# Kernel optimization log

Hardware: AMD Instinct MI355X
Metric: run time of the kernel (lower is better)

The kernel has to match this reference:

```python
import jax, jax.numpy as jnp
import numpy as np
from jax.scipy.linalg import expm, solve_triangular

B, N, K, A, V = 2, 256, 16, 16, 32000
ALPHA = 1.0
LAMBDA_BELIEF = 1.0
EPS = 1e-8   # kl_divergence jitter
EPS2 = 1e-6  # pairwise-KL jitter


def _spd(key, b, n, k, scale=0.3):
    a = jax.random.normal(key, (b, n, k, k)) * scale
    return jnp.einsum('bnkl,bnml->bnkm', a, a) + jnp.eye(k)


def setup_inputs() -> dict:
    key = jax.random.key(0)
    ks = jax.random.split(key, 9)
    mu = jax.random.normal(ks[0], (B, N, K))
    Sigma = _spd(ks[1], B, N, K)
    phi = jax.random.normal(ks[2], (B, N, A)) * 0.05
    mu_prior = jax.random.normal(ks[3], (B, N, K))
    Sigma_prior = _spd(ks[4], B, N, K)
    beta = jax.random.uniform(ks[5], (B, N, N)) / N
    W_out = jax.random.normal(ks[6], (V, K)) * 0.02
    R = jax.random.normal(ks[7], (A, K, K))
    generators = (R - jnp.swapaxes(R, -1, -2)) * 0.1  # skew-symmetric Lie generators
    targets = jax.random.randint(ks[8], (B, N), 0, V)
    return {"mu": mu, "Sigma": Sigma, "phi": phi, "mu_prior": mu_prior,
            "Sigma_prior": Sigma_prior, "beta": beta, "W_out": W_out,
            "generators": generators, "targets": targets}


def _bexpm(M):
    # batched matrix exponential over leading dims
    shape = M.shape
    return jax.vmap(expm)(M.reshape(-1, shape[-2], shape[-1])).reshape(shape)


def _potential(mu, Sigma, phi, mu_prior, Sigma_prior, beta, W_out, generators, targets):
    I = jnp.eye(K, dtype=mu.dtype)

    # --- V_self: alpha * sum_n KL(q_n || p_n), explicit-inverse formulation ---
    Sq = Sigma + EPS * I
    Sp = Sigma_prior + EPS * I
    Sp_inv = jnp.linalg.inv(Sp)
    trace_t = jnp.einsum('bnij,bnji->bn', Sp_inv, Sq)
    dmu = mu_prior - mu
    mahal = jnp.einsum('bni,bnij,bnj->bn', dmu, Sp_inv, dmu)
    logdet = jnp.linalg.slogdet(Sp)[1] - jnp.linalg.slogdet(Sq)[1]
    kl_self = 0.5 * (trace_t + mahal - K + logdet)
    V_self = ALPHA * kl_self.sum(-1)

    # --- V_align: pairwise KL under Lie transport Omega_ij = e^{phi_i G} e^{-phi_j G} ---
    phi_mat = jnp.einsum('bna,aij->bnij', phi, generators)          # (B,N,K,K)
    exp_phi = _bexpm(phi_mat)
    exp_neg_phi = _bexpm(-phi_mat)
    Omega = jnp.einsum('bikl,bjlm->bijkm', exp_phi, exp_neg_phi)    # (B,N,N,K,K)
    mu_t = jnp.einsum('bijkl,bjl->bijk', Omega, mu)                 # (B,N,N,K)
    # Omega Sigma_j Omega^T (congruence -> SPD)
    Sigma_t = jnp.einsum('bijkl,bjlm,bijnm->bijkn', Omega, Sigma, Omega)

    Stp = Sigma_t + EPS2 * I
    L_p = jnp.linalg.cholesky(Stp)                                  # (B,N,N,K,K)
    Sigma_i = jnp.broadcast_to((Sigma + EPS2 * I)[:, :, None], (B, N, N, K, K))
    Y = solve_triangular(L_p, Sigma_i, lower=True)
    Z = solve_triangular(jnp.swapaxes(L_p, -1, -2), Y, lower=False)
    trace_term = jnp.diagonal(Z, axis1=-2, axis2=-1).sum(-1)        # (B,N,N)

    delta = mu_t - mu[:, :, None, :]
    v = solve_triangular(L_p, delta[..., None], lower=True)[..., 0]
    mahal_term = (v ** 2).sum(-1)

    logdet_p = 2.0 * jnp.log(jnp.diagonal(L_p, axis1=-2, axis2=-1) + EPS2).sum(-1)
    L_q = jnp.linalg.cholesky(Sigma + EPS2 * I)                     # (B,N,K,K)
    logdet_q = 2.0 * jnp.log(jnp.diagonal(L_q, axis1=-2, axis2=-1) + EPS2).sum(-1)

    kl_all = 0.5 * (trace_term + mahal_term - K + logdet_p - logdet_q[:, :, None])
    kl_all = jnp.maximum(kl_all, 0.0)
    kl_all = kl_all * (1.0 - jnp.eye(N, dtype=mu.dtype))            # zero diagonal
    V_align = LAMBDA_BELIEF * (beta * kl_all).sum((-2, -1))

    # --- V_ce: cross entropy over W_out projection of mu ---
    logits = jnp.einsum('bnk,vk->bnv', mu, W_out)
    logp = jax.nn.log_softmax(logits, axis=-1)
    ce = -jnp.take_along_axis(logp, targets[..., None], axis=-1)[..., 0]
    V_ce = ce.sum(-1)

    return V_self + V_align + V_ce


def reference(mu, Sigma, phi, mu_prior, Sigma_prior, beta, W_out, generators, targets):
    return _potential(mu, Sigma, phi, mu_prior, Sigma_prior, beta, W_out, generators, targets)
```

## Files before the change

kernel.cpp:

```cpp
#include <hip/hip_runtime.h>
#include <math.h>

#define NB 2
#define NN 256
#define KD 16
#define VV 32000
#define EPS_SELF 1e-8f
#define EPS_AL   1e-6f
#define NNODES (NB*NN)

#define CE_ROWS 8
#define CE_CH   32
#define CE_CHUNK (VV/CE_CH)

#define OFF_MT  0
#define OFF_SH  (NNODES*16)
#define OFF_P   (OFF_SH + NNODES*256)
#define OFF_LD  (OFF_P + NNODES*256)
#define OFF_KLS (OFF_LD + NNODES)
#define OFF_AP  (OFF_KLS + NNODES)
#define OFF_CEP (OFF_AP + NNODES)
#define OFF_CNT (OFF_CEP + NNODES*CE_CH)
#define WS_FLOATS (OFF_CNT + 4)

#define WAVE_SYNC() asm volatile("s_waitcnt lgkmcnt(0)" ::: "memory")

__device__ __forceinline__ void ld4(float* dst, const float4 v) {
  dst[0] = v.x; dst[1] = v.y; dst[2] = v.z; dst[3] = v.w;
}

__device__ __forceinline__ float dot16a(const float* a, const float* b) {
  float acc = 0.f;
  #pragma unroll
  for (int j = 0; j < 16; ++j) acc = fmaf(a[j], b[j], acc);
  return acc;
}

__device__ __forceinline__ void gj16(float aq[4], const int g, const int c, float* ldacc) {
  #pragma unroll
  for (int k = 0; k < 16; ++k) {
    float d    = __shfl(aq[k & 3], ((k >> 2) << 4) | k);
    float rowk = __shfl(aq[k & 3], ((k >> 2) << 4) | c);
    float ck[4];
    #pragma unroll
    for (int q = 0; q < 4; ++q) ck[q] = __shfl(aq[q], (g << 4) | k);
    if (ldacc) *ldacc += logf(d);
    float dinv = 1.f / d;
    #pragma unroll
    for (int q = 0; q < 4; ++q) {
      int r = 4*g + q;
      float vgen = fmaf(-ck[q] * dinv, rowk, aq[q]);
      aq[q] = (r == k) ? ((c == k) ? dinv : aq[q] * dinv)
                       : ((c == k) ? (-ck[q] * dinv) : vgen);
    }
  }
}

template<int QUIRK>
__device__ __forceinline__ float ge16_logdet(float aq[4], const int g, const int c) {
  float ld = 0.f;
  #pragma unroll
  for (int k = 0; k < 16; ++k) {
    float d    = __shfl(aq[k & 3], ((k >> 2) << 4) | k);
    float rowk = __shfl(aq[k & 3], ((k >> 2) << 4) | c);
    float ck[4];
    #pragma unroll
    for (int q = 0; q < 4; ++q) ck[q] = __shfl(aq[q], (g << 4) | k);
    ld += QUIRK ? 2.f * logf(sqrtf(d) + EPS_AL) : logf(d);
    float dinv = 1.f / d;
    #pragma unroll
    for (int q = 0; q < 4; ++q) {
      int r = 4*g + q;
      float upd = fmaf(-ck[q] * dinv, rowk, aq[q]);
      aq[q] = (r > k && c > k) ? upd : aq[q];
    }
  }
  return ld;
}

#define DOT16(q0,q1,q2,q3,A) \
  fmaf(q0.x,A[0],fmaf(q0.y,A[1],fmaf(q0.z,A[2],fmaf(q0.w,A[3], \
  fmaf(q1.x,A[4],fmaf(q1.y,A[5],fmaf(q1.z,A[6],fmaf(q1.w,A[7], \
  fmaf(q2.x,A[8],fmaf(q2.y,A[9],fmaf(q2.z,A[10],fmaf(q2.w,A[11], \
  fmaf(q3.x,A[12],fmaf(q3.y,A[13],fmaf(q3.z,A[14],q3.w*A[15])))))))))))))))

__global__ __launch_bounds__(256) void fusedA_kernel(
    const float* __restrict__ mu, const float* __restrict__ Sigma,
    const float* __restrict__ phi, const float* __restrict__ mu_prior,
    const float* __restrict__ Sigma_prior, const float* __restrict__ gen,
    const float* __restrict__ W, float* __restrict__ ws)
{
  __shared__ __align__(16) float smem[4][980];
  const int tid = threadIdx.x;
  const int bid = blockIdx.x;

  if (bid < 256) {
    if (bid == 0 && tid == 0) *(unsigned*)(ws + OFF_CNT) = 0u;
    const int w = tid >> 6, l = tid & 63;
    const int g = l >> 4, c = l & 15;
    const int unit = bid * 4 + w;
    const int role = unit & 1, node = unit >> 1;
    float* COLp = &smem[w][0];
    float* ROWp = &smem[w][320];
    float* AUXp = &smem[w][640];

    if (role == 0) {
      float phis[16];
      {
        const float4* p4 = (const float4*)(phi + node*16);
        ld4(phis, p4[0]); ld4(phis+4, p4[1]); ld4(phis+8, p4[2]); ld4(phis+12, p4[3]);
      }
      float x[4] = {0.f, 0.f, 0.f, 0.f};
      #pragma unroll
      for (int aa = 0; aa < 16; ++aa) {
        float4 gq = *(const float4*)(gen + aa*256 + c*16 + 4*g);
        x[0] = fmaf(phis[aa], gq.x, x[0]);
        x[1] = fmaf(phis[aa], gq.y, x[1]);
        x[2] = fmaf(phis[aa], gq.z, x[2]);
        x[3] = fmaf(phis[aa], gq.w, x[3]);
      }
      #pragma unroll
      for (int q = 0; q < 4; ++q) x[q] *= -0.125f;

      #pragma unroll
      for (int q = 0; q < 4; ++q) ROWp[(4*g+q)*20 + c] = x[q];
      WAVE_SYNC();
      float Mrow[4][16];
      #pragma unroll
      for (int q = 0; q < 4; ++q)
        #pragma unroll
        for (int j4 = 0; j4 < 4; ++j4)
          ld4(&Mrow[q][4*j4], *(const float4*)&ROWp[(4*g+q)*20 + 4*j4]);

      float t[4];
      #pragma unroll
      for (int q = 0; q < 4; ++q) t[q] = ((4*g+q) == c ? 1.f : 0.f) + x[q]*0.125f;
      for (int k = 7; k >= 1; --k) {
        *(float4*)&COLp[c*20 + 4*g] = make_float4(t[0], t[1], t[2], t[3]);
        WAVE_SYNC();
        float T[16];
        #pragma unroll
        for (int j4 = 0; j4 < 4; ++j4) ld4(&T[4*j4], *(const float4*)&COLp[c*20 + 4*j4]);
        #pragma unroll
        for (int q = 0; q < 4; ++q)
          t[q] = ((4*g+q) == c ? 1.f : 0.f) + dot16a(Mrow[q], T) / (float)k;
      }
      for (int s = 0; s < 3; ++s) {
        *(float4*)&COLp[c*20 + 4*g] = make_float4(t[0], t[1], t[2], t[3]);
        #pragma unroll
        for (int q = 0; q < 4; ++q) ROWp[(4*g+q)*20 + c] = t[q];
        WAVE_SYNC();
        float T[16];
        #pragma unroll
        for (int j4 = 0; j4 < 4; ++j4) ld4(&T[4*j4], *(const float4*)&COLp[c*20 + 4*j4]);
        float nt[4];
        #pragma unroll
        for (int q = 0; q < 4; ++q) {
          float acc = 0.f;
          #pragma unroll
          for (int j4 = 0; j4 < 4; ++j4) {
            float4 rv = *(const float4*)&ROWp[(4*g+q)*20 + 4*j4];
            acc = fmaf(rv.x, T[4*j4+0], acc);
            acc = fmaf(rv.y, T[4*j4+1], acc);
            acc = fmaf(rv.z, T[4*j4+2], acc);
            acc = fmaf(rv.w, T[4*j4+3], acc);
          }
          nt[q] = acc;
        }
        #pragma unroll
        for (int q = 0; q < 4; ++q) t[q] = nt[q];
      }
      *(float4*)&COLp[c*20 + 4*g] = make_float4(t[0], t[1], t[2], t[3]);
      WAVE_SYNC();
      float Ecol[16];
      #pragma unroll
      for (int j4 = 0; j4 < 4; ++j4) ld4(&Ecol[4*j4], *(const float4*)&COLp[c*20 + 4*j4]);

      float w1q[4];
      #pragma unroll
      for (int q = 0; q < 4; ++q) {
        float S[16];
        const float4* s4 = (const float4*)(Sigma + node*256 + (4*g+q)*16);
        ld4(S, s4[0]); ld4(S+4, s4[1]); ld4(S+8, s4[2]); ld4(S+12, s4[3]);
        w1q[q] = dot16a(S, Ecol);
      }
      *(float4*)&AUXp[c*20 + 4*g] = make_float4(w1q[0], w1q[1], w1q[2], w1q[3]);
      WAVE_SYNC();
      float W1c[16];
      #pragma unroll
      for (int j4 = 0; j4 < 4; ++j4) ld4(&W1c[4*j4], *(const float4*)&AUXp[c*20 + 4*j4]);

      float sh[4];
      #pragma unroll
      for (int q = 0; q < 4; ++q) {
        float Er[16];
        #pragma unroll
        for (int j4 = 0; j4 < 4; ++j4) ld4(&Er[4*j4], *(const float4*)&COLp[(4*g+q)*20 + 4*j4]);
        sh[q] = dot16a(Er, W1c) + ((4*g+q) == c ? EPS_AL : 0.f);
      }
      *(float4*)(ws + OFF_SH + node*256 + c*16 + 4*g) = make_float4(sh[0], sh[1], sh[2], sh[3]);

      {
        float muv[16];
        const float4* m4 = (const float4*)(mu + node*16);
        ld4(muv, m4[0]); ld4(muv+4, m4[1]); ld4(muv+8, m4[2]); ld4(muv+12, m4[3]);
        float mt = dot16a(Ecol, muv);
        if (g == 0) ws[OFF_MT + node*16 + c] = mt;
      }
      gj16(sh, g, c, (float*)nullptr);
      *(float4*)(ws + OFF_P + node*256 + c*16 + 4*g) = make_float4(sh[0], sh[1], sh[2], sh[3]);
    } else {
      float sp[4];
      {
        float4 v = *(const float4*)(Sigma_prior + node*256 + c*16 + 4*g);
        sp[0] = v.x + ((4*g+0 == c) ? EPS_SELF : 0.f);
        sp[1] = v.y + ((4*g+1 == c) ? EPS_SELF : 0.f);
        sp[2] = v.z + ((4*g+2 == c) ? EPS_SELF : 0.f);
        sp[3] = v.w + ((4*g+3 == c) ? EPS_SELF : 0.f);
      }
      float ldSp = 0.f;
      gj16(sp, g, c, &ldSp);

      float dmur[4], dmuc;
      {
        float4 a = *(const float4*)(mu_prior + node*16 + 4*g);
        float4 b = *(const float4*)(mu + node*16 + 4*g);
        dmur[0] = a.x - b.x; dmur[1] = a.y - b.y; dmur[2] = a.z - b.z; dmur[3] = a.w - b.w;
        dmuc = mu_prior[node*16 + c] - mu[node*16 + c];
      }
      float4 sv = *(const float4*)(Sigma + node*256 + c*16 + 4*g);
      float val = 0.f;
      {
        float s0 = sv.x + ((4*g+0 == c) ? EPS_SELF : 0.f);
        float s1 = sv.y + ((4*g+1 == c) ? EPS_SELF : 0.f);
        float s2 = sv.z + ((4*g+2 == c) ? EPS_SELF : 0.f);
        float s3 = sv.w + ((4*g+3 == c) ? EPS_SELF : 0.f);
        val = fmaf(sp[0], s0 + dmur[0]*dmuc, val);
        val = fmaf(sp[1], s1 + dmur[1]*dmuc, val);
        val = fmaf(sp[2], s2 + dmur[2]*dmuc, val);
        val = fmaf(sp[3], s3 + dmur[3]*dmuc, val);
      }
      #pragma unroll
      for (int o = 32; o; o >>= 1) val += __shfl_xor(val, o);

      float sq[4];
      sq[0] = sv.x + ((4*g+0 == c) ? EPS_SELF : 0.f);
      sq[1] = sv.y + ((4*g+1 == c) ? EPS_SELF : 0.f);
      sq[2] = sv.z + ((4*g+2 == c) ? EPS_SELF : 0.f);
      sq[3] = sv.w + ((4*g+3 == c) ? EPS_SELF : 0.f);
      float ldSq = ge16_logdet<0>(sq, g, c);
      float sg[4];
      sg[0] = sv.x + ((4*g+0 == c) ? EPS_AL : 0.f);
      sg[1] = sv.y + ((4*g+1 == c) ? EPS_AL : 0.f);
      sg[2] = sv.z + ((4*g+2 == c) ? EPS_AL : 0.f);
      sg[3] = sv.w + ((4*g+3 == c) ? EPS_AL : 0.f);
      float ldq = ge16_logdet<1>(sg, g, c);
      if (l == 0) {
        ws[OFF_KLS + node] = 0.5f * (val - 16.f + ldSp - ldSq);
        ws[OFF_LD + node]  = ldq;
      }
    }
  } else {
    const int idx = bid - 256;
    const int grp = idx & 63;
    const int ch  = idx >> 6;
    const int row0 = grp * CE_ROWS;
    float* mu_s = &smem[0][0];
    float* wred = &smem[0][128];

    if (tid < CE_ROWS*16) mu_s[tid] = mu[row0*16 + tid];
    __syncthreads();

    float A[CE_ROWS][16];
    #pragma unroll
    for (int r = 0; r < CE_ROWS; ++r)
      #pragma unroll
      for (int k = 0; k < 16; ++k) A[r][k] = mu_s[r*16+k];

    float acc[CE_ROWS];
    #pragma unroll
    for (int r = 0; r < CE_ROWS; ++r) acc[r] = 0.f;

    const float4* W4 = (const float4*)W;
    const int v0 = ch * CE_CHUNK;
    for (int v = v0 + tid; v < v0 + CE_CHUNK; v += 256) {
      float4 q0 = W4[v*4+0], q1 = W4[v*4+1], q2 = W4[v*4+2], q3 = W4[v*4+3];
      #pragma unroll
      for (int r = 0; r < CE_ROWS; ++r) {
        float lg = DOT16(q0,q1,q2,q3,A[r]);
        acc[r] += __expf(lg);
      }
    }
    #pragma unroll
    for (int r = 0; r < CE_ROWS; ++r)
      #pragma unroll
      for (int o = 32; o; o >>= 1) acc[r] += __shfl_xor(acc[r], o);
    const int w = tid >> 6, l = tid & 63;
    if (l == 0) {
      #pragma unroll
      for (int r = 0; r < CE_ROWS; ++r) wred[w*CE_ROWS + r] = acc[r];
    }
    __syncthreads();
    if (tid < CE_ROWS)
      ws[OFF_CEP + (row0 + tid)*CE_CH + ch] =
          wred[tid] + wred[CE_ROWS + tid] + wred[2*CE_ROWS + tid] + wred[3*CE_ROWS + tid];
  }
}

#define PSTR 260
__global__ __launch_bounds__(256) void alignB_kernel(
    const float* __restrict__ beta, const float* __restrict__ mu,
    const float* __restrict__ W, const int* __restrict__ targets,
    float* __restrict__ ws, float* __restrict__ out)
{
  __shared__ __align__(16) float ShI[16*PSTR];
  __shared__ __align__(16) float PJ[16*PSTR];
  __shared__ float mtI[256], mtJ[256], ldI[16], ldJ[16], red[4];
  __shared__ int lastflag;
  const int tid = threadIdx.x;
  const int ti = tid & 15, tj = tid >> 4;
  const int bx = blockIdx.x & 15, by = (blockIdx.x >> 4) & 15, bz = blockIdx.x >> 8;
  const int nodeI0 = bz*256 + by*16, nodeJ0 = bz*256 + bx*16;

  for (int idx = tid; idx < 16*256; idx += 256) {
    int row = idx >> 8, col = idx & 255;
    ShI[row*PSTR + col] = ws[OFF_SH + (nodeI0 + row)*256 + col];
    PJ [row*PSTR + col] = ws[OFF_P  + (nodeJ0 + row)*256 + col];
  }
  mtI[tid] = ws[OFF_MT + nodeI0*16 + tid];
  mtJ[tid] = ws[OFF_MT + nodeJ0*16 + tid];
  if (tid < 16) { ldI[tid] = ws[OFF_LD + nodeI0 + tid]; ldJ[tid] = ws[OFF_LD + nodeJ0 + tid]; }
  __syncthreads();

  const float4* si4 = (const float4*)&ShI[ti*PSTR];
  const float4* pj4 = (const float4*)&PJ[tj*PSTR];
  float tr = 0.f;
  #pragma unroll 16
  for (int t = 0; t < 64; ++t) {
    float4 xv = si4[t], yv = pj4[t];
    tr = fmaf(xv.x, yv.x, tr);
    tr = fmaf(xv.y, yv.y, tr);
    tr = fmaf(xv.z, yv.z, tr);
    tr = fmaf(xv.w, yv.w, tr);
  }

  const float* pj = &PJ[tj*PSTR];
  float d[16];
  #pragma unroll
  for (int k = 0; k < 16; ++k) d[k] = mtJ[tj*16+k] - mtI[ti*16+k];
  float mah = 0.f;
  #pragma unroll
  for (int k = 0; k < 16; ++k) {
    float acc = 0.f;
    #pragma unroll
    for (int ll = 0; ll < 16; ++ll) acc = fmaf(pj[k*16+ll], d[ll], acc);
    mah = fmaf(d[k], acc, mah);
  }

  float kl = 0.5f * (tr + mah - 16.f + ldJ[tj] - ldI[ti]);
  kl = fmaxf(kl, 0.f);
  int gi = by*16 + ti, gj = bx*16 + tj;
  float contrib = (gi == gj) ? 0.f : kl * beta[bz*65536 + gi*256 + gj];
  #pragma unroll
  for (int o = 32; o; o >>= 1) contrib += __shfl_down(contrib, o);
  __syncthreads();
  if ((tid & 63) == 0) red[tid >> 6] = contrib;
  __syncthreads();
  if (tid == 0) {
    ws[OFF_AP + (bz*16 + by)*16 + bx] = red[0] + red[1] + red[2] + red[3];
    unsigned old = __hip_atomic_fetch_add((unsigned*)(ws + OFF_CNT), 1u,
                                          __ATOMIC_ACQ_REL, __HIP_MEMORY_SCOPE_AGENT);
    lastflag = (old == 511u);
  }
  __syncthreads();

  if (lastflag) {
    double* dred = (double*)ShI;
    double v[2];
    #pragma unroll
    for (int b = 0; b < 2; ++b) {
      int row = b*256 + tid;
      float s = 0.f;
      #pragma unroll
      for (int c2 = 0; c2 < CE_CH; ++c2) s += ws[OFF_CEP + row*CE_CH + c2];
      int t = targets[row];
      float dt = 0.f;
      const float4* wt4 = (const float4*)(W + t*16);
      const float4* mr4 = (const float4*)(mu + row*16);
      #pragma unroll
      for (int j4 = 0; j4 < 4; ++j4) {
        float4 a = mr4[j4], bb = wt4[j4];
        dt = fmaf(a.x, bb.x, dt); dt = fmaf(a.y, bb.y, dt);
        dt = fmaf(a.z, bb.z, dt); dt = fmaf(a.w, bb.w, dt);
      }
      double ce = (double)logf(s) - (double)dt;
      v[b] = (double)ws[OFF_KLS + row] + (double)ws[OFF_AP + row] + ce;
    }
    for (int b = 0; b < 2; ++b) {
      dred[tid] = v[b];
      __syncthreads();
      for (int h = 128; h > 0; h >>= 1) {
        if (tid < h) dred[tid] += dred[tid + h];
        __syncthreads();
      }
      if (tid == 0) out[b] = (float)dred[0];
      __syncthreads();
    }
  }
}

extern "C" void kernel_launch(void* const* d_in, const int* in_sizes, int n_in,
                              void* d_out, int out_size, void* d_ws, size_t ws_size,
                              hipStream_t stream) {
  const float* mu          = (const float*)d_in[0];
  const float* Sigma       = (const float*)d_in[1];
  const float* phi         = (const float*)d_in[2];
  const float* mu_prior    = (const float*)d_in[3];
  const float* Sigma_prior = (const float*)d_in[4];
  const float* beta        = (const float*)d_in[5];
  const float* W_out       = (const float*)d_in[6];
  const float* gen         = (const float*)d_in[7];
  const int*   targets     = (const int*)d_in[8];
  float* out = (float*)d_out;
  float* ws  = (float*)d_ws;
  if (ws_size < (size_t)WS_FLOATS * sizeof(float)) return;

  fusedA_kernel<<<256 + (NNODES/CE_ROWS)*CE_CH, 256, 0, stream>>>(
      mu, Sigma, phi, mu_prior, Sigma_prior, gen, W_out, ws);
  alignB_kernel<<<NB*16*16, 256, 0, stream>>>(beta, mu, W_out, targets, ws, out);
}
```

Measured before the change: 44.32 us.

## Fold pairwise Mahalanobis term into trace via precomputed rank-one and projections

```diff
diff --git a/kernel.cpp b/kernel.cpp
--- a/kernel.cpp
+++ b/kernel.cpp
@@ -14,12 +14,14 @@
 #define CE_CHUNK (VV/CE_CH)
 
 #define OFF_MT  0
-#define OFF_SH  (NNODES*16)
-#define OFF_P   (OFF_SH + NNODES*256)
+#define OFF_O   (NNODES*16)
+#define OFF_P   (OFF_O + NNODES*256)
 #define OFF_LD  (OFF_P + NNODES*256)
 #define OFF_KLS (OFF_LD + NNODES)
 #define OFF_AP  (OFF_KLS + NNODES)
-#define OFF_CEP (OFF_AP + NNODES)
+#define OFF_Y   (OFF_AP + NNODES)
+#define OFF_W   (OFF_Y + NNODES*16)
+#define OFF_CEP (OFF_W + NNODES)
 #define OFF_CNT (OFF_CEP + NNODES*CE_CH)
 #define WS_FLOATS (OFF_CNT + 4)
 
@@ -34,6 +36,10 @@
   #pragma unroll
   for (int j = 0; j < 16; ++j) acc = fmaf(a[j], b[j], acc);
   return acc;
+}
+
+__device__ __forceinline__ float dot4(float4 a, float4 b) {
+  return fmaf(a.x, b.x, fmaf(a.y, b.y, fmaf(a.z, b.z, a.w * b.w)));
 }
 
 __device__ __forceinline__ void gj16(float aq[4], const int g, const int c, float* ldacc) {
@@ -78,13 +84,7 @@
   return ld;
 }
 
-#define DOT16(q0,q1,q2,q3,A) \
-  fmaf(q0.x,A[0],fmaf(q0.y,A[1],fmaf(q0.z,A[2],fmaf(q0.w,A[3], \
-  fmaf(q1.x,A[4],fmaf(q1.y,A[5],fmaf(q1.z,A[6],fmaf(q1.w,A[7], \
-  fmaf(q2.x,A[8],fmaf(q2.y,A[9],fmaf(q2.z,A[10],fmaf(q2.w,A[11], \
-  fmaf(q3.x,A[12],fmaf(q3.y,A[13],fmaf(q3.z,A[14],q3.w*A[15])))))))))))))))
-
-__global__ __launch_bounds__(256) void fusedA_kernel(
+__global__ __launch_bounds__(256, 1) void fusedA_kernel(
     const float* __restrict__ mu, const float* __restrict__ Sigma,
     const float* __restrict__ phi, const float* __restrict__ mu_prior,
     const float* __restrict__ Sigma_prior, const float* __restrict__ gen,
@@ -198,17 +198,34 @@
         for (int j4 = 0; j4 < 4; ++j4) ld4(&Er[4*j4], *(const float4*)&COLp[(4*g+q)*20 + 4*j4]);
         sh[q] = dot16a(Er, W1c) + ((4*g+q) == c ? EPS_AL : 0.f);
       }
-      *(float4*)(ws + OFF_SH + node*256 + c*16 + 4*g) = make_float4(sh[0], sh[1], sh[2], sh[3]);
-
+
+      float mtc;
       {
         float muv[16];
         const float4* m4 = (const float4*)(mu + node*16);
         ld4(muv, m4[0]); ld4(muv+4, m4[1]); ld4(muv+8, m4[2]); ld4(muv+12, m4[3]);
-        float mt = dot16a(Ecol, muv);
-        if (g == 0) ws[OFF_MT + node*16 + c] = mt;
-      }
+        mtc = dot16a(Ecol, muv);
+      }
+      float mt4[4];
+      #pragma unroll
+      for (int q = 0; q < 4; ++q) mt4[q] = __shfl(mtc, 4*g + q);
+
+      *(float4*)(ws + OFF_O + node*256 + c*16 + 4*g) =
+          make_float4(fmaf(mt4[0], mtc, sh[0]), fmaf(mt4[1], mtc, sh[1]),
+                      fmaf(mt4[2], mtc, sh[2]), fmaf(mt4[3], mtc, sh[3]));
+      if (g == 0) ws[OFF_MT + node*16 + c] = mtc;
+
       gj16(sh, g, c, (float*)nullptr);
       *(float4*)(ws + OFF_P + node*256 + c*16 + 4*g) = make_float4(sh[0], sh[1], sh[2], sh[3]);
+
+      float part = sh[0]*mt4[0] + sh[1]*mt4[1] + sh[2]*mt4[2] + sh[3]*mt4[3];
+      part += __shfl_xor(part, 16);
+      part += __shfl_xor(part, 32);
+      if (g == 0) ws[OFF_Y + node*16 + c] = part;
+      float wv = mtc * part;
+      wv += __shfl_xor(wv, 1); wv += __shfl_xor(wv, 2);
+      wv += __shfl_xor(wv, 4); wv += __shfl_xor(wv, 8);
+      if (l == 0) ws[OFF_W + node] = wv;
     } else {
       float sp[4];
       {
@@ -265,17 +282,17 @@
     const int grp = idx & 63;
     const int ch  = idx >> 6;
     const int row0 = grp * CE_ROWS;
-    float* mu_s = &smem[0][0];
-    float* wred = &smem[0][128];
-
-    if (tid < CE_ROWS*16) mu_s[tid] = mu[row0*16 + tid];
-    __syncthreads();
-
-    float A[CE_ROWS][16];
-    #pragma unroll
-    for (int r = 0; r < CE_ROWS; ++r)
-      #pragma unroll
-      for (int k = 0; k < 16; ++k) A[r][k] = mu_s[r*16+k];
+    float* wred = &smem[0][0];
+
+    const float4* M4 = (const float4*)(mu + row0*16);
+    float4 R0a=M4[0],  R0b=M4[1],  R0c=M4[2],  R0d=M4[3];
+    float4 R1a=M4[4],  R1b=M4[5],  R1c=M4[6],  R1d=M4[7];
+    float4 R2a=M4[8],  R2b=M4[9],  R2c=M4[10], R2d=M4[11];
+    float4 R3a=M4[12], R3b=M4[13], R3c=M4[14], R3d=M4[15];
+    float4 R4a=M4[16], R4b=M4[17], R4c=M4[18], R4d=M4[19];
+    float4 R5a=M4[20], R5b=M4[21], R5c=M4[22], R5d=M4[23];
+    float4 R6a=M4[24], R6b=M4[25], R6c=M4[26], R6d=M4[27];
+    float4 R7a=M4[28], R7b=M4[29], R7c=M4[30], R7d=M4[31];
 
     float acc[CE_ROWS];
     #pragma unroll
@@ -285,11 +302,9 @@
     const int v0 = ch * CE_CHUNK;
     for (int v = v0 + tid; v < v0 + CE_CHUNK; v += 256) {
       float4 q0 = W4[v*4+0], q1 = W4[v*4+1], q2 = W4[v*4+2], q3 = W4[v*4+3];
-      #pragma unroll
-      for (int r = 0; r < CE_ROWS; ++r) {
-        float lg = DOT16(q0,q1,q2,q3,A[r]);
-        acc[r] += __expf(lg);
-      }
+      #define CE_ROW(n) acc[n] += __expf(dot4(q0,R##n##a) + dot4(q1,R##n##b) + dot4(q2,R##n##c) + dot4(q3,R##n##d));
+      CE_ROW(0) CE_ROW(1) CE_ROW(2) CE_ROW(3) CE_ROW(4) CE_ROW(5) CE_ROW(6) CE_ROW(7)
+      #undef CE_ROW
     }
     #pragma unroll
     for (int r = 0; r < CE_ROWS; ++r)
@@ -313,9 +328,11 @@
     const float* __restrict__ W, const int* __restrict__ targets,
     float* __restrict__ ws, float* __restrict__ out)
 {
-  __shared__ __align__(16) float ShI[16*PSTR];
+  __shared__ __align__(16) float OI[16*PSTR];
   __shared__ __align__(16) float PJ[16*PSTR];
-  __shared__ float mtI[256], mtJ[256], ldI[16], ldJ[16], red[4];
+  __shared__ __align__(16) float mtI[256];
+  __shared__ __align__(16) float yJ[256];
+  __shared__ float wJ[16], ldI[16], ldJ[16], red[4];
   __shared__ int lastflag;
   const int tid = threadIdx.x;
   const int ti = tid & 15, tj = tid >> 4;
@@ -324,40 +341,35 @@
 
   for (int idx = tid; idx < 16*256; idx += 256) {
     int row = idx >> 8, col = idx & 255;
-    ShI[row*PSTR + col] = ws[OFF_SH + (nodeI0 + row)*256 + col];
-    PJ [row*PSTR + col] = ws[OFF_P  + (nodeJ0 + row)*256 + col];
+    OI[row*PSTR + col] = ws[OFF_O + (nodeI0 + row)*256 + col];
+    PJ[row*PSTR + col] = ws[OFF_P + (nodeJ0 + row)*256 + col];
   }
   mtI[tid] = ws[OFF_MT + nodeI0*16 + tid];
-  mtJ[tid] = ws[OFF_MT + nodeJ0*16 + tid];
-  if (tid < 16) { ldI[tid] = ws[OFF_LD + nodeI0 + tid]; ldJ[tid] = ws[OFF_LD + nodeJ0 + tid]; }
+  yJ[tid]  = ws[OFF_Y  + nodeJ0*16 + tid];
+  if (tid < 16) {
+    wJ[tid]  = ws[OFF_W  + nodeJ0 + tid];
+    ldI[tid] = ws[OFF_LD + nodeI0 + tid];
+    ldJ[tid] = ws[OFF_LD + nodeJ0 + tid];
+  }
   __syncthreads();
 
-  const float4* si4 = (const float4*)&ShI[ti*PSTR];
+  const float4* oi4 = (const float4*)&OI[ti*PSTR];
   const float4* pj4 = (const float4*)&PJ[tj*PSTR];
   float tr = 0.f;
   #pragma unroll 16
   for (int t = 0; t < 64; ++t) {
-    float4 xv = si4[t], yv = pj4[t];
+    float4 xv = oi4[t], yv = pj4[t];
     tr = fmaf(xv.x, yv.x, tr);
     tr = fmaf(xv.y, yv.y, tr);
     tr = fmaf(xv.z, yv.z, tr);
     tr = fmaf(xv.w, yv.w, tr);
   }
-
-  const float* pj = &PJ[tj*PSTR];
-  float d[16];
-  #pragma unroll
-  for (int k = 0; k < 16; ++k) d[k] = mtJ[tj*16+k] - mtI[ti*16+k];
-  float mah = 0.f;
-  #pragma unroll
-  for (int k = 0; k < 16; ++k) {
-    float acc = 0.f;
-    #pragma unroll
-    for (int ll = 0; ll < 16; ++ll) acc = fmaf(pj[k*16+ll], d[ll], acc);
-    mah = fmaf(d[k], acc, mah);
-  }
-
-  float kl = 0.5f * (tr + mah - 16.f + ldJ[tj] - ldI[ti]);
+  const float4* mi4 = (const float4*)&mtI[ti*16];
+  const float4* yj4 = (const float4*)&yJ[tj*16];
+  float diy = dot4(mi4[0], yj4[0]) + dot4(mi4[1], yj4[1])
+            + dot4(mi4[2], yj4[2]) + dot4(mi4[3], yj4[3]);
+
+  float kl = 0.5f * (tr + wJ[tj] - 2.f*diy - 16.f + ldJ[tj] - ldI[ti]);
   kl = fmaxf(kl, 0.f);
   int gi = by*16 + ti, gj = bx*16 + tj;
   float contrib = (gi == gj) ? 0.f : kl * beta[bz*65536 + gi*256 + gj];
@@ -375,7 +387,7 @@
   __syncthreads();
 
   if (lastflag) {
-    double* dred = (double*)ShI;
+    double* dred = (double*)OI;
     double v[2];
     #pragma unroll
     for (int b = 0; b < 2; ++b) {
```

Measured after the change: 58.03 us. 30.9% more time.
